# Kernel tuning notes

Measured on AMD Instinct MI355X. Metric: run time of the kernel, lower is better.

## Reference

```python
import jax, jax.numpy as jnp
import numpy as np

NFEAT = 128
NHID = 64
NLAYER = 3
N_NODES = 50000
N_EDGES = 800000
N_GRAPHS = 512
BN_EPS = 1e-5


def _bn(x, gamma, beta):
    # BatchNorm1d in training mode: biased batch stats over the node axis.
    m = x.mean(axis=0)
    v = x.var(axis=0)
    return (x - m) * jax.lax.rsqrt(v + BN_EPS) * gamma + beta


def _pool(x, batch):
    # global_mean_pool: segment mean over graph ids.
    s = jax.ops.segment_sum(x, batch, num_segments=N_GRAPHS)
    c = jax.ops.segment_sum(jnp.ones((x.shape[0], 1), x.dtype), batch, num_segments=N_GRAPHS)
    return s / jnp.maximum(c, 1.0)


def setup_inputs() -> dict:
    key = jax.random.key(0)
    ks = jax.random.split(key, 16)
    x = jax.random.normal(ks[0], (N_NODES, NFEAT), dtype=jnp.float32)
    edge_index = jax.random.randint(ks[1], (2, N_EDGES), 0, N_NODES, dtype=jnp.int64)
    batch = jnp.sort(jax.random.randint(ks[2], (N_NODES,), 0, N_GRAPHS, dtype=jnp.int64))
    s_in = 1.0 / np.sqrt(NFEAT)
    s_h = 1.0 / np.sqrt(NHID)
    return {
        "x": x,
        "edge_index": edge_index,
        "batch": batch,
        "Wt": jax.random.uniform(ks[3], (NFEAT, NHID), jnp.float32, -s_in, s_in),
        "bt": jax.random.uniform(ks[4], (NHID,), jnp.float32, -s_in, s_in),
        "gt": jnp.ones((NHID,), jnp.float32),
        "bet": jnp.zeros((NHID,), jnp.float32),
        "W1": jax.random.uniform(ks[5], (NLAYER, NHID, NHID), jnp.float32, -s_h, s_h),
        "b1": jax.random.uniform(ks[6], (NLAYER, NHID), jnp.float32, -s_h, s_h),
        "W2": jax.random.uniform(ks[7], (NLAYER, NHID, NHID), jnp.float32, -s_h, s_h),
        "b2": jax.random.uniform(ks[8], (NLAYER, NHID), jnp.float32, -s_h, s_h),
        "g": jnp.ones((NLAYER, NHID), jnp.float32),
        "be": jnp.zeros((NLAYER, NHID), jnp.float32),
    }


def reference(x, edge_index, batch, Wt, bt, gt, bet, W1, b1, W2, b2, g, be):
    n = x.shape[0]
    src, dst = edge_index[0], edge_index[1]
    # input transform: Linear + BN
    h = _bn(x @ Wt + bt, gt, bet)
    embeds = [_pool(h, batch)]
    for l in range(NLAYER):
        # GINConv, eps=0: mlp(x_i + sum_{j->i} x_j); flow source->target
        agg = jax.ops.segment_sum(h[src], dst, num_segments=n)
        z = h + agg
        z = jax.nn.relu(z @ W1[l] + b1[l]) @ W2[l] + b2[l]
        h = jax.nn.relu(_bn(z, g[l], be[l]))
        embeds.append(_pool(h, batch))
    return jnp.stack(embeds)  # [NLAYER+1, N_GRAPHS, NHID]
```

## Files before the change

kernel.cpp:

```cpp
#include <hip/hip_runtime.h>

#define NFEAT   128
#define NHID    64
#define NLAYER  3
#define NNODES  50000
#define NEDGES  800000
#define NGRAPHS 512
#define BN_EPS  1e-5f
#define MLPB    1563
#define CAP     64
#define PADW    68
#define FILLB   2048
#define SETUPB  83

typedef unsigned short u16;
typedef __attribute__((ext_vector_type(8))) short bf8;
typedef __attribute__((ext_vector_type(4))) float f32x4;

__device__ inline float b2f(u16 v) { return __uint_as_float(((unsigned)v) << 16); }
__device__ inline u16 f2b(float f) {
    unsigned u = __float_as_uint(f);
    return (u16)((u + 0x7FFF + ((u >> 16) & 1)) >> 16);
}
__device__ inline bf8 ldb8(const u16* p) {
    union { uint2 a[2]; bf8 v; } u;
    u.a[0] = *(const uint2*)p;
    u.a[1] = *(const uint2*)(p + 4);
    return u.v;
}
__device__ inline bf8 ldb8g(const u16* p) {
    union { uint4 a; bf8 v; } u;
    u.a = *(const uint4*)p;
    return u.v;
}
__device__ inline void add8(float* a, const uint4 v) {
    a[0] += __uint_as_float(v.x << 16);
    a[1] += __uint_as_float(v.x & 0xFFFF0000u);
    a[2] += __uint_as_float(v.y << 16);
    a[3] += __uint_as_float(v.y & 0xFFFF0000u);
    a[4] += __uint_as_float(v.z << 16);
    a[5] += __uint_as_float(v.z & 0xFFFF0000u);
    a[6] += __uint_as_float(v.w << 16);
    a[7] += __uint_as_float(v.w & 0xFFFF0000u);
}
__device__ inline void unp8(float* a, const uint4 v) {
    a[0] = __uint_as_float(v.x << 16);
    a[1] = __uint_as_float(v.x & 0xFFFF0000u);
    a[2] = __uint_as_float(v.y << 16);
    a[3] = __uint_as_float(v.y & 0xFFFF0000u);
    a[4] = __uint_as_float(v.z << 16);
    a[5] = __uint_as_float(v.z & 0xFFFF0000u);
    a[6] = __uint_as_float(v.w << 16);
    a[7] = __uint_as_float(v.w & 0xFFFF0000u);
}
__device__ inline uint2 pack4(float a, float b, float c, float d) {
    uint2 r;
    r.x = (unsigned)f2b(a) | ((unsigned)f2b(b) << 16);
    r.y = (unsigned)f2b(c) | ((unsigned)f2b(d) << 16);
    return r;
}

__global__ __launch_bounds__(256) void k_build(const int* __restrict__ ei,
                                               int* __restrict__ deg,
                                               u16* __restrict__ col,
                                               const float* __restrict__ Wt,
                                               const float* __restrict__ W1,
                                               const float* __restrict__ W2,
                                               const int* __restrict__ batch,
                                               u16* __restrict__ wtin,
                                               u16* __restrict__ wt,
                                               int* __restrict__ gstart) {
    int tid = threadIdx.x;
    if (blockIdx.x < FILLB) {
        int rangeId = blockIdx.x & 7, chunk = blockIdx.x >> 3;
        int lo = rangeId * (NNODES / 8), hi = lo + (NNODES / 8);
        int ebeg = chunk * (NEDGES / 256), eend = ebeg + (NEDGES / 256);
        int e = ebeg + tid;
        for (; e + 7 * 256 < eend; e += 8 * 256) {
            int d[8];
#pragma unroll
            for (int i = 0; i < 8; ++i) d[i] = ei[NEDGES + e + i * 256];
#pragma unroll
            for (int i = 0; i < 8; ++i) {
                if (d[i] >= lo && d[i] < hi) {
                    int s = atomicAdd(&deg[d[i]], 1);
                    if (s < CAP) col[d[i] * CAP + s] = (u16)ei[e + i * 256];
                }
            }
        }
        for (; e < eend; e += 256) {
            int dst = ei[NEDGES + e];
            if (dst >= lo && dst < hi) {
                int s = atomicAdd(&deg[dst], 1);
                if (s < CAP) col[dst * CAP + s] = (u16)ei[e];
            }
        }
        return;
    }
    int idx = (blockIdx.x - FILLB) * 256 + tid;
    if (idx < NFEAT * NHID) {
        int n = idx >> 7, k = idx & 127;
        wtin[n * NFEAT + k] = f2b(Wt[k * NHID + n]);
        return;
    }
    idx -= NFEAT * NHID;
    if (idx < NLAYER * NHID * NHID) {
        int l = idx >> 12, rem = idx & 4095, n = rem >> 6, k = rem & 63;
        wt[l * 8192 + n * 64 + k]        = f2b(W1[l * 4096 + k * 64 + n]);
        wt[l * 8192 + 4096 + n * 64 + k] = f2b(W2[l * 4096 + k * 64 + n]);
        return;
    }
    idx -= NLAYER * NHID * NHID;
    if (idx <= NGRAPHS) {
        if (idx == NGRAPHS) { gstart[NGRAPHS] = NNODES; return; }
        int lo = 0, hi = NNODES;
        while (lo < hi) {
            int mid = (lo + hi) >> 1;
            if (batch[mid] < idx) lo = mid + 1; else hi = mid;
        }
        gstart[idx] = lo;
    }
}

__global__ __launch_bounds__(256) void k_gemm_in(const float* __restrict__ x,
                                                 const u16* __restrict__ wtin,
                                                 const float* __restrict__ bt,
                                                 u16* __restrict__ zout,
                                                 float* __restrict__ partials) {
    __shared__ u16 sx[32][132];
    __shared__ float ps[128];
    int tid = threadIdx.x;
    int base = blockIdx.x * 32;
#pragma unroll
    for (int i = 0; i < 4; ++i) {
        int idx = i * 256 + tid;
        int row = idx >> 5, kq = idx & 31;
        int rc = min(base + row, NNODES - 1);
        float4 v = ((const float4*)(x + (long long)rc * NFEAT))[kq];
        *(uint2*)&sx[row][kq * 4] = pack4(v.x, v.y, v.z, v.w);
    }
    __syncthreads();
    int w = tid >> 6, lane = tid & 63;
    int m = lane & 15, g = lane >> 4;
    int ncol = w * 16 + m;
    bool hiv = (base + 16 < NNODES);
    float bb = bt[ncol];
    f32x4 cl = {bb, bb, bb, bb}, ch = {bb, bb, bb, bb};
    const u16* wn = wtin + ncol * NFEAT;
#pragma unroll
    for (int s = 0; s < 4; ++s) {
        int k0 = s * 32 + g * 8;
        bf8 B  = ldb8g(wn + k0);
        bf8 Al = ldb8(&sx[m][k0]);
        bf8 Ah = ldb8(&sx[16 + m][k0]);
        cl = __builtin_amdgcn_mfma_f32_16x16x32_bf16(Al, B, cl, 0, 0, 0);
        ch = __builtin_amdgcn_mfma_f32_16x16x32_bf16(Ah, B, ch, 0, 0, 0);
    }
    float s1 = cl[0] + cl[1] + cl[2] + cl[3];
    float s2 = cl[0] * cl[0] + cl[1] * cl[1] + cl[2] * cl[2] + cl[3] * cl[3];
    if (hiv) {
        s1 += ch[0] + ch[1] + ch[2] + ch[3];
        s2 += ch[0] * ch[0] + ch[1] * ch[1] + ch[2] * ch[2] + ch[3] * ch[3];
    }
    s1 += __shfl_xor(s1, 16, 64); s1 += __shfl_xor(s1, 32, 64);
    s2 += __shfl_xor(s2, 16, 64); s2 += __shfl_xor(s2, 32, 64);
    if (lane < 16) {
        ps[w * 16 + lane] = s1;
        ps[64 + w * 16 + lane] = s2;
    }
#pragma unroll
    for (int i = 0; i < 4; ++i) {
        zout[(base + g * 4 + i) * NHID + ncol] = f2b(cl[i]);
        if (hiv) zout[(base + 16 + g * 4 + i) * NHID + ncol] = f2b(ch[i]);
    }
    __syncthreads();
    if (tid < 128) partials[blockIdx.x * 128 + tid] = ps[tid];
}

__global__ __launch_bounds__(256) void k_red(const float* __restrict__ partials,
                                             float* __restrict__ stats, int np) {
    __shared__ float red[4];
    int c = blockIdx.x, t = threadIdx.x;
    float s = 0.f;
    for (int i = t; i < np; i += 256) s += partials[i * 128 + c];
#pragma unroll
    for (int off = 32; off >= 1; off >>= 1) s += __shfl_xor(s, off, 64);
    if ((t & 63) == 0) red[t >> 6] = s;
    __syncthreads();
    if (t == 0) stats[c] = red[0] + red[1] + red[2] + red[3];
}

__global__ __launch_bounds__(256) void k_bnh(const u16* __restrict__ z,
                                             const float* __restrict__ stats,
                                             const float* __restrict__ gamma,
                                             const float* __restrict__ beta,
                                             u16* __restrict__ h) {
    int idx = blockIdx.x * 256 + threadIdx.x;
    if (idx >= NNODES * NHID / 8) return;
    int j0 = (idx & 7) * 8;
    uint4 v = ((const uint4*)z)[idx];
    float o[8];
    unp8(o, v);
#pragma unroll
    for (int k = 0; k < 8; ++k) {
        int j = j0 + k;
        float m = stats[j] * (1.0f / NNODES);
        float var = stats[64 + j] * (1.0f / NNODES) - m * m;
        float sc = rsqrtf(var + BN_EPS) * gamma[j];
        o[k] = fmaxf(fmaf(o[k], sc, beta[j] - m * sc), 0.f);
    }
    uint4 w;
    uint2 p0 = pack4(o[0], o[1], o[2], o[3]);
    uint2 p1 = pack4(o[4], o[5], o[6], o[7]);
    w.x = p0.x; w.y = p0.y; w.z = p1.x; w.w = p1.y;
    ((uint4*)h)[idx] = w;
}

__global__ __launch_bounds__(256) void k_poolfin(const u16* __restrict__ z,
                                                 const float* __restrict__ stats,
                                                 const float* __restrict__ gamma,
                                                 const float* __restrict__ beta,
                                                 const int* __restrict__ gstart,
                                                 const float* __restrict__ poolacc,
                                                 float* __restrict__ out) {
    if (blockIdx.x >= NGRAPHS) {
        int idx = (int)(blockIdx.x - NGRAPHS) * 256 + threadIdx.x;
        if (idx < NLAYER * NGRAPHS * NHID) {
            int g = (idx >> 6) & (NGRAPHS - 1);
            float cnt = (float)(gstart[g + 1] - gstart[g]);
            out[idx] = poolacc[idx] / fmaxf(cnt, 1.0f);
        }
        return;
    }
    __shared__ float4 red[4][16];
    int gph = blockIdx.x;
    int lane = threadIdx.x & 63, w = threadIdx.x >> 6;
    int c = lane & 15, ws = lane >> 4;
    int slot = w * 4 + ws;
    int j0 = c * 4;
    float sc[4], sh[4];
#pragma unroll
    for (int k = 0; k < 4; ++k) {
        int j = j0 + k;
        float m = stats[j] * (1.0f / NNODES);
        float var = stats[64 + j] * (1.0f / NNODES) - m * m;
        sc[k] = rsqrtf(var + BN_EPS) * gamma[j];
        sh[k] = beta[j] - m * sc[k];
    }
    const ushort4* z4 = (const ushort4*)z;
    int s0 = gstart[gph], e0 = gstart[gph + 1];
    float a[4] = {0.f, 0.f, 0.f, 0.f};
    for (int r = s0 + slot; r < e0; r += 16) {
        ushort4 v = z4[r * 16 + c];
        a[0] += fmaxf(fmaf(b2f(v.x), sc[0], sh[0]), 0.f);
        a[1] += fmaxf(fmaf(b2f(v.y), sc[1], sh[1]), 0.f);
        a[2] += fmaxf(fmaf(b2f(v.z), sc[2], sh[2]), 0.f);
        a[3] += fmaxf(fmaf(b2f(v.w), sc[3], sh[3]), 0.f);
    }
#pragma unroll
    for (int k = 0; k < 4; ++k) {
        a[k] += __shfl_xor(a[k], 16, 64);
        a[k] += __shfl_xor(a[k], 32, 64);
    }
    if (lane < 16) red[w][c] = make_float4(a[0], a[1], a[2], a[3]);
    __syncthreads();
    if (threadIdx.x < 16) {
        float4 r0 = red[0][threadIdx.x], r1 = red[1][threadIdx.x];
        float4 r2 = red[2][threadIdx.x], r3 = red[3][threadIdx.x];
        float inv = 1.0f / fmaxf((float)(e0 - s0), 1.0f);
        float* o = &out[NLAYER * NGRAPHS * NHID + gph * NHID + threadIdx.x * 4];
        o[0] = (r0.x + r1.x + r2.x + r3.x) * inv;
        o[1] = (r0.y + r1.y + r2.y + r3.y) * inv;
        o[2] = (r0.z + r1.z + r2.z + r3.z) * inv;
        o[3] = (r0.w + r1.w + r2.w + r3.w) * inv;
    }
}

template <int AFFINE>
__global__ __launch_bounds__(256) void k_mlp(const u16* __restrict__ hin,
                                             const float* __restrict__ stats,
                                             const float* __restrict__ gamma,
                                             const float* __restrict__ beta,
                                             const int* __restrict__ batch,
                                             const int* __restrict__ deg,
                                             const u16* __restrict__ col,
                                             const u16* __restrict__ w1t,
                                             const float* __restrict__ b1,
                                             const u16* __restrict__ w2t,
                                             const float* __restrict__ b2,
                                             u16* __restrict__ zout,
                                             float* __restrict__ partials,
                                             float* __restrict__ poolacc) {
    __shared__ u16 szb[32][PADW];
    __shared__ u16 stb[32][PADW];
    __shared__ float ps[128];
    int tid = threadIdx.x;
    int w = tid >> 6, lane = tid & 63;
    int nd = lane >> 3, c8 = lane & 7;
    int node = w * 8 + nd;
    int base = blockIdx.x * 32;
    int r = base + node;
    bool rv = (r < NNODES);
    int rc = rv ? r : (NNODES - 1);
    const uint4* h16 = (const uint4*)hin;

    float sc[8], sh[8];
    if (AFFINE) {
#pragma unroll
        for (int k = 0; k < 8; ++k) {
            int j = c8 * 8 + k;
            float m = stats[j] * (1.0f / NNODES);
            float var = stats[64 + j] * (1.0f / NNODES) - m * m;
            sc[k] = rsqrtf(var + BN_EPS) * gamma[j];
            sh[k] = beta[j] - m * sc[k];
        }
    }

    float acc[8], acc2[8] = {0, 0, 0, 0, 0, 0, 0, 0};
    float selfh[8];
    {
        uint4 sv = h16[rc * 8 + c8];
        unp8(acc, sv);
#pragma unroll
        for (int k = 0; k < 8; ++k)
            selfh[k] = AFFINE ? fmaf(acc[k], sc[k], sh[k]) : acc[k];
    }
    int dd = rv ? min(deg[r], CAP) : 0;
    {
        const u16* cp = col + rc * CAP;
        int t = 0;
        for (; t + 8 <= dd; t += 8) {
            uint4 iv = *(const uint4*)(cp + t);
            int s0 = iv.x & 0xFFFF, s1 = iv.x >> 16;
            int s2 = iv.y & 0xFFFF, s3 = iv.y >> 16;
            int s4 = iv.z & 0xFFFF, s5 = iv.z >> 16;
            int s6 = iv.w & 0xFFFF, s7 = iv.w >> 16;
            uint4 v0 = h16[s0 * 8 + c8];
            uint4 v1 = h16[s1 * 8 + c8];
            uint4 v2 = h16[s2 * 8 + c8];
            uint4 v3 = h16[s3 * 8 + c8];
            uint4 v4 = h16[s4 * 8 + c8];
            uint4 v5 = h16[s5 * 8 + c8];
            uint4 v6 = h16[s6 * 8 + c8];
            uint4 v7 = h16[s7 * 8 + c8];
            add8(acc, v0); add8(acc2, v1); add8(acc, v2); add8(acc2, v3);
            add8(acc, v4); add8(acc2, v5); add8(acc, v6); add8(acc2, v7);
        }
        if (t + 4 <= dd) {
            uint2 iv = *(const uint2*)(cp + t);
            int s0 = iv.x & 0xFFFF, s1 = iv.x >> 16;
            int s2 = iv.y & 0xFFFF, s3 = iv.y >> 16;
            uint4 v0 = h16[s0 * 8 + c8];
            uint4 v1 = h16[s1 * 8 + c8];
            uint4 v2 = h16[s2 * 8 + c8];
            uint4 v3 = h16[s3 * 8 + c8];
            add8(acc, v0); add8(acc2, v1); add8(acc, v2); add8(acc2, v3);
            t += 4;
        }
        for (; t < dd; ++t) {
            uint4 v0 = h16[(int)cp[t] * 8 + c8];
            add8(acc, v0);
        }
    }
    {
        float zv[8];
#pragma unroll
        for (int k = 0; k < 8; ++k) {
            float s = acc[k] + acc2[k];
            zv[k] = AFFINE ? fmaf(s, sc[k], (float)(1 + dd) * sh[k]) : s;
            if (!rv) zv[k] = 0.f;
        }
        *(uint2*)&szb[node][c8 * 8]     = pack4(zv[0], zv[1], zv[2], zv[3]);
        *(uint2*)&szb[node][c8 * 8 + 4] = pack4(zv[4], zv[5], zv[6], zv[7]);
    }

    int m = lane & 15, g = lane >> 4;
    int ncol = w * 16 + m;
    const u16* w1n = w1t + ncol * 64;
    const u16* w2n = w2t + ncol * 64;
    bf8 B0 = ldb8g(w1n + g * 8);
    bf8 B1 = ldb8g(w1n + 32 + g * 8);
    bf8 D0 = ldb8g(w2n + g * 8);
    bf8 D1 = ldb8g(w2n + 32 + g * 8);

    {
        int r0 = base + w * 8;
        int myg = rv ? batch[r] : -1;
        int g_lo = batch[min(r0, NNODES - 1)];
        int g_hi = batch[min(r0 + 7, NNODES - 1)];
        for (int gg = g_lo; gg <= g_hi; ++gg) {
            float v[8];
#pragma unroll
            for (int k = 0; k < 8; ++k) {
                v[k] = (myg == gg) ? selfh[k] : 0.f;
                v[k] += __shfl_xor(v[k], 8, 64);
                v[k] += __shfl_xor(v[k], 16, 64);
                v[k] += __shfl_xor(v[k], 32, 64);
            }
            if (lane < 8) {
                float* p = &poolacc[gg * NHID + lane * 8];
#pragma unroll
                for (int k = 0; k < 8; ++k) atomicAdd(p + k, v[k]);
            }
        }
    }
    __syncthreads();

    bool hiv = (base + 16 < NNODES);
    bf8 Al0 = ldb8(&szb[m][g * 8]);
    bf8 Al1 = ldb8(&szb[m][32 + g * 8]);
    bf8 Ah0 = ldb8(&szb[16 + m][g * 8]);
    bf8 Ah1 = ldb8(&szb[16 + m][32 + g * 8]);
    float bb1 = b1[ncol];
    f32x4 cl = {bb1, bb1, bb1, bb1}, ch = {bb1, bb1, bb1, bb1};
    cl = __builtin_amdgcn_mfma_f32_16x16x32_bf16(Al0, B0, cl, 0, 0, 0);
    cl = __builtin_amdgcn_mfma_f32_16x16x32_bf16(Al1, B1, cl, 0, 0, 0);
    ch = __builtin_amdgcn_mfma_f32_16x16x32_bf16(Ah0, B0, ch, 0, 0, 0);
    ch = __builtin_amdgcn_mfma_f32_16x16x32_bf16(Ah1, B1, ch, 0, 0, 0);
#pragma unroll
    for (int i = 0; i < 4; ++i) {
        stb[g * 4 + i][ncol]      = f2b(fmaxf(cl[i], 0.f));
        stb[16 + g * 4 + i][ncol] = f2b(fmaxf(ch[i], 0.f));
    }
    __syncthreads();

    bf8 Cl0 = ldb8(&stb[m][g * 8]);
    bf8 Cl1 = ldb8(&stb[m][32 + g * 8]);
    bf8 Ch0 = ldb8(&stb[16 + m][g * 8]);
    bf8 Ch1 = ldb8(&stb[16 + m][32 + g * 8]);
    float bb2 = b2[ncol];
    f32x4 el = {bb2, bb2, bb2, bb2}, eh = {bb2, bb2, bb2, bb2};
    el = __builtin_amdgcn_mfma_f32_16x16x32_bf16(Cl0, D0, el, 0, 0, 0);
    el = __builtin_amdgcn_mfma_f32_16x16x32_bf16(Cl1, D1, el, 0, 0, 0);
    eh = __builtin_amdgcn_mfma_f32_16x16x32_bf16(Ch0, D0, eh, 0, 0, 0);
    eh = __builtin_amdgcn_mfma_f32_16x16x32_bf16(Ch1, D1, eh, 0, 0, 0);

    float s1 = el[0] + el[1] + el[2] + el[3];
    float s2 = el[0] * el[0] + el[1] * el[1] + el[2] * el[2] + el[3] * el[3];
    if (hiv) {
        s1 += eh[0] + eh[1] + eh[2] + eh[3];
        s2 += eh[0] * eh[0] + eh[1] * eh[1] + eh[2] * eh[2] + eh[3] * eh[3];
    }
    s1 += __shfl_xor(s1, 16, 64); s1 += __shfl_xor(s1, 32, 64);
    s2 += __shfl_xor(s2, 16, 64); s2 += __shfl_xor(s2, 32, 64);
    if (lane < 16) {
        ps[w * 16 + lane] = s1;
        ps[64 + w * 16 + lane] = s2;
    }
#pragma unroll
    for (int i = 0; i < 4; ++i) {
        zout[(base + g * 4 + i) * NHID + ncol] = f2b(el[i]);
        if (hiv) zout[(base + 16 + g * 4 + i) * NHID + ncol] = f2b(eh[i]);
    }
    __syncthreads();
    if (tid < 128) partials[blockIdx.x * 128 + tid] = ps[tid];
}

extern "C" void kernel_launch(void* const* d_in, const int* in_sizes, int n_in,
                              void* d_out, int out_size, void* d_ws, size_t ws_size,
                              hipStream_t stream) {
    const float* x     = (const float*)d_in[0];
    const int*   ei    = (const int*)d_in[1];
    const int*   batch = (const int*)d_in[2];
    const float* Wt    = (const float*)d_in[3];
    const float* bt    = (const float*)d_in[4];
    const float* gt    = (const float*)d_in[5];
    const float* bet   = (const float*)d_in[6];
    const float* W1    = (const float*)d_in[7];
    const float* b1    = (const float*)d_in[8];
    const float* W2    = (const float*)d_in[9];
    const float* b2    = (const float*)d_in[10];
    const float* g     = (const float*)d_in[11];
    const float* be    = (const float*)d_in[12];
    float* out = (float*)d_out;

    u16* A          = (u16*)d_ws;
    u16* B          = A + NNODES * NHID;
    u16* H          = B + NNODES * NHID;
    u16* wt         = H + NNODES * NHID;
    u16* wtin       = wt + NLAYER * 2 * NHID * NHID;
    float* partials = (float*)(wtin + NFEAT * NHID);
    float* stats    = partials + MLPB * 128;
    int* deg        = (int*)(stats + 4 * 128);
    float* poolacc  = (float*)(deg + NNODES);
    u16* col        = (u16*)(poolacc + NLAYER * NGRAPHS * NHID);
    int* gstart     = (int*)(col + NNODES * CAP);

    size_t zbytes = NNODES * sizeof(int) + NLAYER * NGRAPHS * NHID * sizeof(float);
    hipMemsetAsync(deg, 0, zbytes, stream);

    k_build<<<FILLB + SETUPB, 256, 0, stream>>>(ei, deg, col, Wt, W1, W2, batch,
                                                wtin, wt, gstart);

    k_gemm_in<<<MLPB, 256, 0, stream>>>(x, wtin, bt, A, partials);
    k_red<<<128, 256, 0, stream>>>(partials, stats, MLPB);

    k_mlp<1><<<MLPB, 256, 0, stream>>>(A, stats, gt, bet, batch, deg, col,
                                       wt, b1, wt + 4096, b2,
                                       B, partials, poolacc);
    k_red<<<128, 256, 0, stream>>>(partials, stats + 128, MLPB);

    k_bnh<<<MLPB, 256, 0, stream>>>(B, stats + 128, g, be, H);
    k_mlp<0><<<MLPB, 256, 0, stream>>>(H, stats + 128, g, be, batch, deg, col,
                                       wt + 8192, b1 + NHID, wt + 8192 + 4096, b2 + NHID,
                                       A, partials, poolacc + NGRAPHS * NHID);
    k_red<<<128, 256, 0, stream>>>(partials, stats + 256, MLPB);

    k_bnh<<<MLPB, 256, 0, stream>>>(A, stats + 256, g + NHID, be + NHID, H);
    k_mlp<0><<<MLPB, 256, 0, stream>>>(H, stats + 256, g + NHID, be + NHID, batch, deg, col,
                                       wt + 16384, b1 + 2 * NHID, wt + 16384 + 4096, b2 + 2 * NHID,
                                       B, partials, poolacc + 2 * NGRAPHS * NHID);
    k_red<<<128, 256, 0, stream>>>(partials, stats + 384, MLPB);

    k_poolfin<<<NGRAPHS + (NLAYER * NGRAPHS * NHID + 255) / 256, 256, 0, stream>>>(
        B, stats + 384, g + 2 * NHID, be + 2 * NHID, gstart, poolacc, out);
}
```

Baseline: 194.6 us.

## Double k_mlp threads to 512, splitting gather and MFMA work per node

k_mlp now launches 512 threads per 32-node block instead of 256. Each node's 64 features are gathered by 16 lanes with 8-byte loads instead of 8 lanes with 16-byte loads, so twice as many independent gather streams are in flight per block. The MFMA stage is split so each of the 8 waves handles one 16-row half and one 16-column group, and the BN partial sums are combined across the two halves in shared memory. The aim is more memory-level parallelism in the latency-bound neighbor gather, at the cost of narrower loads, more threads, and one extra shared-memory reduction step.

```diff
diff --git a/kernel.cpp b/kernel.cpp
--- a/kernel.cpp
+++ b/kernel.cpp
@@ -33,15 +33,17 @@
     u.a = *(const uint4*)p;
     return u.v;
 }
-__device__ inline void add8(float* a, const uint4 v) {
+__device__ inline void add4(float* a, const uint2 v) {
     a[0] += __uint_as_float(v.x << 16);
     a[1] += __uint_as_float(v.x & 0xFFFF0000u);
     a[2] += __uint_as_float(v.y << 16);
     a[3] += __uint_as_float(v.y & 0xFFFF0000u);
-    a[4] += __uint_as_float(v.z << 16);
-    a[5] += __uint_as_float(v.z & 0xFFFF0000u);
-    a[6] += __uint_as_float(v.w << 16);
-    a[7] += __uint_as_float(v.w & 0xFFFF0000u);
+}
+__device__ inline void unp4(float* a, const uint2 v) {
+    a[0] = __uint_as_float(v.x << 16);
+    a[1] = __uint_as_float(v.x & 0xFFFF0000u);
+    a[2] = __uint_as_float(v.y << 16);
+    a[3] = __uint_as_float(v.y & 0xFFFF0000u);
 }
 __device__ inline void unp8(float* a, const uint4 v) {
     a[0] = __uint_as_float(v.x << 16);
@@ -277,7 +279,7 @@
 }
 
 template <int AFFINE>
-__global__ __launch_bounds__(256) void k_mlp(const u16* __restrict__ hin,
+__global__ __launch_bounds__(512) void k_mlp(const u16* __restrict__ hin,
                                              const float* __restrict__ stats,
                                              const float* __restrict__ gamma,
                                              const float* __restrict__ beta,
@@ -293,22 +295,22 @@
                                              float* __restrict__ poolacc) {
     __shared__ u16 szb[32][PADW];
     __shared__ u16 stb[32][PADW];
-    __shared__ float ps[128];
+    __shared__ float ps2[2][128];
     int tid = threadIdx.x;
     int w = tid >> 6, lane = tid & 63;
-    int nd = lane >> 3, c8 = lane & 7;
-    int node = w * 8 + nd;
+    int nq = lane >> 4, c = lane & 15;
+    int node = w * 4 + nq;
     int base = blockIdx.x * 32;
     int r = base + node;
     bool rv = (r < NNODES);
     int rc = rv ? r : (NNODES - 1);
-    const uint4* h16 = (const uint4*)hin;
-
-    float sc[8], sh[8];
+    const uint2* h8 = (const uint2*)hin;
+
+    float sc[4], sh[4];
     if (AFFINE) {
 #pragma unroll
-        for (int k = 0; k < 8; ++k) {
-            int j = c8 * 8 + k;
+        for (int k = 0; k < 4; ++k) {
+            int j = c * 4 + k;
             float m = stats[j] * (1.0f / NNODES);
             float var = stats[64 + j] * (1.0f / NNODES) - m * m;
             sc[k] = rsqrtf(var + BN_EPS) * gamma[j];
@@ -316,13 +318,13 @@
         }
     }
 
-    float acc[8], acc2[8] = {0, 0, 0, 0, 0, 0, 0, 0};
-    float selfh[8];
+    float acc[4], acc2[4] = {0, 0, 0, 0};
+    float selfh[4];
     {
-        uint4 sv = h16[rc * 8 + c8];
-        unp8(acc, sv);
-#pragma unroll
-        for (int k = 0; k < 8; ++k)
+        uint2 sv = h8[rc * 16 + c];
+        unp4(acc, sv);
+#pragma unroll
+        for (int k = 0; k < 4; ++k)
             selfh[k] = AFFINE ? fmaf(acc[k], sc[k], sh[k]) : acc[k];
     }
     int dd = rv ? min(deg[r], CAP) : 0;
@@ -335,47 +337,47 @@
             int s2 = iv.y & 0xFFFF, s3 = iv.y >> 16;
             int s4 = iv.z & 0xFFFF, s5 = iv.z >> 16;
             int s6 = iv.w & 0xFFFF, s7 = iv.w >> 16;
-            uint4 v0 = h16[s0 * 8 + c8];
-            uint4 v1 = h16[s1 * 8 + c8];
-            uint4 v2 = h16[s2 * 8 + c8];
-            uint4 v3 = h16[s3 * 8 + c8];
-            uint4 v4 = h16[s4 * 8 + c8];
-            uint4 v5 = h16[s5 * 8 + c8];
-            uint4 v6 = h16[s6 * 8 + c8];
-            uint4 v7 = h16[s7 * 8 + c8];
-            add8(acc, v0); add8(acc2, v1); add8(acc, v2); add8(acc2, v3);
-            add8(acc, v4); add8(acc2, v5); add8(acc, v6); add8(acc2, v7);
+            uint2 v0 = h8[s0 * 16 + c];
+            uint2 v1 = h8[s1 * 16 + c];
+            uint2 v2 = h8[s2 * 16 + c];
+            uint2 v3 = h8[s3 * 16 + c];
+            uint2 v4 = h8[s4 * 16 + c];
+            uint2 v5 = h8[s5 * 16 + c];
+            uint2 v6 = h8[s6 * 16 + c];
+            uint2 v7 = h8[s7 * 16 + c];
+            add4(acc, v0); add4(acc2, v1); add4(acc, v2); add4(acc2, v3);
+            add4(acc, v4); add4(acc2, v5); add4(acc, v6); add4(acc2, v7);
         }
         if (t + 4 <= dd) {
             uint2 iv = *(const uint2*)(cp + t);
             int s0 = iv.x & 0xFFFF, s1 = iv.x >> 16;
             int s2 = iv.y & 0xFFFF, s3 = iv.y >> 16;
-            uint4 v0 = h16[s0 * 8 + c8];
-            uint4 v1 = h16[s1 * 8 + c8];
-            uint4 v2 = h16[s2 * 8 + c8];
-            uint4 v3 = h16[s3 * 8 + c8];
-            add8(acc, v0); add8(acc2, v1); add8(acc, v2); add8(acc2, v3);
+            uint2 v0 = h8[s0 * 16 + c];
+            uint2 v1 = h8[s1 * 16 + c];
+            uint2 v2 = h8[s2 * 16 + c];
+            uint2 v3 = h8[s3 * 16 + c];
+            add4(acc, v0); add4(acc2, v1); add4(acc, v2); add4(acc2, v3);
             t += 4;
         }
         for (; t < dd; ++t) {
-            uint4 v0 = h16[(int)cp[t] * 8 + c8];
-            add8(acc, v0);
+            uint2 v0 = h8[(int)cp[t] * 16 + c];
+            add4(acc, v0);
         }
     }
     {
-        float zv[8];
-#pragma unroll
-        for (int k = 0; k < 8; ++k) {
+        float zv[4];
+#pragma unroll
+        for (int k = 0; k < 4; ++k) {
             float s = acc[k] + acc2[k];
             zv[k] = AFFINE ? fmaf(s, sc[k], (float)(1 + dd) * sh[k]) : s;
             if (!rv) zv[k] = 0.f;
         }
-        *(uint2*)&szb[node][c8 * 8]     = pack4(zv[0], zv[1], zv[2], zv[3]);
-        *(uint2*)&szb[node][c8 * 8 + 4] = pack4(zv[4], zv[5], zv[6], zv[7]);
+        *(uint2*)&szb[node][c * 4] = pack4(zv[0], zv[1], zv[2], zv[3]);
     }
 
     int m = lane & 15, g = lane >> 4;
-    int ncol = w * 16 + m;
+    int half = w >> 2, cg = w & 3;
+    int ncol = cg * 16 + m;
     const u16* w1n = w1t + ncol * 64;
     const u16* w2n = w2t + ncol * 64;
     bf8 B0 = ldb8g(w1n + g * 8);
@@ -384,76 +386,63 @@
     bf8 D1 = ldb8g(w2n + 32 + g * 8);
 
     {
-        int r0 = base + w * 8;
+        int r0 = base + w * 4;
         int myg = rv ? batch[r] : -1;
         int g_lo = batch[min(r0, NNODES - 1)];
-        int g_hi = batch[min(r0 + 7, NNODES - 1)];
+        int g_hi = batch[min(r0 + 3, NNODES - 1)];
         for (int gg = g_lo; gg <= g_hi; ++gg) {
-            float v[8];
-#pragma unroll
-            for (int k = 0; k < 8; ++k) {
+            float v[4];
+#pragma unroll
+            for (int k = 0; k < 4; ++k) {
                 v[k] = (myg == gg) ? selfh[k] : 0.f;
-                v[k] += __shfl_xor(v[k], 8, 64);
                 v[k] += __shfl_xor(v[k], 16, 64);
                 v[k] += __shfl_xor(v[k], 32, 64);
             }
-            if (lane < 8) {
-                float* p = &poolacc[gg * NHID + lane * 8];
-#pragma unroll
-                for (int k = 0; k < 8; ++k) atomicAdd(p + k, v[k]);
+            if (lane < 16) {
+                float* p = &poolacc[gg * NHID + lane * 4];
+#pragma unroll
+                for (int k = 0; k < 4; ++k) atomicAdd(p + k, v[k]);
             }
         }
     }
     __syncthreads();
 
     bool hiv = (base + 16 < NNODES);
-    bf8 Al0 = ldb8(&szb[m][g * 8]);
-    bf8 Al1 = ldb8(&szb[m][32 + g * 8]);
-    bf8 Ah0 = ldb8(&szb[16 + m][g * 8]);
-    bf8 Ah1 = ldb8(&szb[16 + m][32 + g * 8]);
+    bool halfv = (half == 0) || hiv;
+    bf8 A0 = ldb8(&szb[half * 16 + m][g * 8]);
+    bf8 A1 = ldb8(&szb[half * 16 + m][32 + g * 8]);
     float bb1 = b1[ncol];
-    f32x4 cl = {bb1, bb1, bb1, bb1}, ch = {bb1, bb1, bb1, bb1};
-    cl = __builtin_amdgcn_mfma_f32_16x16x32_bf16(Al0, B0, cl, 0, 0, 0);
-    cl = __builtin_amdgcn_mfma_f32_16x16x32_bf16(Al1, B1, cl, 0, 0, 0);
-    ch = __builtin_amdgcn_mfma_f32_16x16x32_bf16(Ah0, B0, ch, 0, 0, 0);
-    ch = __builtin_amdgcn_mfma_f32_16x16x32_bf16(Ah1, B1, ch, 0, 0, 0);
-#pragma unroll
-    for (int i = 0; i < 4; ++i) {
-        stb[g * 4 + i][ncol]      = f2b(fmaxf(cl[i], 0.f));
-        stb[16 + g * 4 + i][ncol] = f2b(fmaxf(ch[i], 0.f));
-    }
-    __syncthreads();
-
-    bf8 Cl0 = ldb8(&stb[m][g * 8]);
-    bf8 Cl1 = ldb8(&stb[m][32 + g * 8]);
-    bf8 Ch0 = ldb8(&stb[16 + m][g * 8]);
-    bf8 Ch1 = ldb8(&stb[16 + m][32 + g * 8]);
+    f32x4 c1 = {bb1, bb1, bb1, bb1};
+    c1 = __builtin_amdgcn_mfma_f32_16x16x32_bf16(A0, B0, c1, 0, 0, 0);
+    c1 = __builtin_amdgcn_mfma_f32_16x16x32_bf16(A1, B1, c1, 0, 0, 0);
+#pragma unroll
+    for (int i = 0; i < 4; ++i)
+        stb[half * 16 + g * 4 + i][ncol] = f2b(fmaxf(c1[i], 0.f));
+    __syncthreads();
+
+    bf8 C0 = ldb8(&stb[half * 16 + m][g * 8]);
+    bf8 C1 = ldb8(&stb[half * 16 + m][32 + g * 8]);
     float bb2 = b2[ncol];
-    f32x4 el = {bb2, bb2, bb2, bb2}, eh = {bb2, bb2, bb2, bb2};
-    el = __builtin_amdgcn_mfma_f32_16x16x32_bf16(Cl0, D0, el, 0, 0, 0);
-    el = __builtin_amdgcn_mfma_f32_16x16x32_bf16(Cl1, D1, el, 0, 0, 0);
-    eh = __builtin_amdgcn_mfma_f32_16x16x32_bf16(Ch0, D0, eh, 0, 0, 0);
-    eh = __builtin_amdgcn_mfma_f32_16x16x32_bf16(Ch1, D1, eh, 0, 0, 0);
-
-    float s1 = el[0] + el[1] + el[2] + el[3];
-    float s2 = el[0] * el[0] + el[1] * el[1] + el[2] * el[2] + el[3] * el[3];
-    if (hiv) {
-        s1 += eh[0] + eh[1] + eh[2] + eh[3];
-        s2 += eh[0] * eh[0] + eh[1] * eh[1] + eh[2] * eh[2] + eh[3] * eh[3];
-    }
+    f32x4 e = {bb2, bb2, bb2, bb2};
+    e = __builtin_amdgcn_mfma_f32_16x16x32_bf16(C0, D0, e, 0, 0, 0);
+    e = __builtin_amdgcn_mfma_f32_16x16x32_bf16(C1, D1, e, 0, 0, 0);
+
+    float s1 = e[0] + e[1] + e[2] + e[3];
+    float s2 = e[0] * e[0] + e[1] * e[1] + e[2] * e[2] + e[3] * e[3];
+    if (!halfv) { s1 = 0.f; s2 = 0.f; }
     s1 += __shfl_xor(s1, 16, 64); s1 += __shfl_xor(s1, 32, 64);
     s2 += __shfl_xor(s2, 16, 64); s2 += __shfl_xor(s2, 32, 64);
     if (lane < 16) {
-        ps[w * 16 + lane] = s1;
-        ps[64 + w * 16 + lane] = s2;
-    }
-#pragma unroll
-    for (int i = 0; i < 4; ++i) {
-        zout[(base + g * 4 + i) * NHID + ncol] = f2b(el[i]);
-        if (hiv) zout[(base + 16 + g * 4 + i) * NHID + ncol] = f2b(eh[i]);
-    }
-    __syncthreads();
-    if (tid < 128) partials[blockIdx.x * 128 + tid] = ps[tid];
+        ps2[half][cg * 16 + lane] = s1;
+        ps2[half][64 + cg * 16 + lane] = s2;
+    }
+    if (halfv) {
+#pragma unroll
+        for (int i = 0; i < 4; ++i)
+            zout[(base + half * 16 + g * 4 + i) * NHID + ncol] = f2b(e[i]);
+    }
+    __syncthreads();
+    if (tid < 128) partials[blockIdx.x * 128 + tid] = ps2[0][tid] + ps2[1][tid];
 }
 
 extern "C" void kernel_launch(void* const* d_in, const int* in_sizes, int n_in,
@@ -495,19 +484,19 @@
     k_gemm_in<<<MLPB, 256, 0, stream>>>(x, wtin, bt, A, partials);
     k_red<<<128, 256, 0, stream>>>(partials, stats, MLPB);
 
-    k_mlp<1><<<MLPB, 256, 0, stream>>>(A, stats, gt, bet, batch, deg, col,
+    k_mlp<1><<<MLPB, 512, 0, stream>>>(A, stats, gt, bet, batch, deg, col,
                                        wt, b1, wt + 4096, b2,
                                        B, partials, poolacc);
     k_red<<<128, 256, 0, stream>>>(partials, stats + 128, MLPB);
 
     k_bnh<<<MLPB, 256, 0, stream>>>(B, stats + 128, g, be, H);
-    k_mlp<0><<<MLPB, 256, 0, stream>>>(H, stats + 128, g, be, batch, deg, col,
+    k_mlp<0><<<MLPB, 512, 0, stream>>>(H, stats + 128, g, be, batch, deg, col,
                                        wt + 8192, b1 + NHID, wt + 8192 + 4096, b2 + NHID,
                                        A, partials, poolacc + NGRAPHS * NHID);
     k_red<<<128, 256, 0, stream>>>(partials, stats + 256, MLPB);
 
     k_bnh<<<MLPB, 256, 0, stream>>>(A, stats + 256, g + NHID, be + NHID, H);
-    k_mlp<0><<<MLPB, 256, 0, stream>>>(H, stats + 256, g + NHID, be + NHID, batch, deg, col,
+    k_mlp<0><<<MLPB, 512, 0, stream>>>(H, stats + 256, g + NHID, be + NHID, batch, deg, col,
                                        wt + 16384, b1 + 2 * NHID, wt + 16384 + 4096, b2 + 2 * NHID,
                                        B, partials, poolacc + 2 * NGRAPHS * NHID);
     k_red<<<128, 256, 0, stream>>>(partials, stats + 384, MLPB);
```

New measurement: 189.3 us. -2.7%, faster.
